# Optimization experiments

Measured on AMD Instinct MI355X. Metric: run time of the kernel, lower is better.

## Reference

```python
import jax, jax.numpy as jnp
import numpy as np

N_NODES = 50000
N_EDGES = 1600000
D_FEAT = 64
N_SCALARS = 4
N_GRAPHS = 64
HIDDEN = 128
OUT = 128


def setup_inputs() -> dict:
    key = jax.random.key(0)
    ks = jax.random.split(key, 8)
    x = jax.random.normal(ks[0], (N_NODES, D_FEAT), dtype=jnp.float32)
    scalars = jax.random.normal(ks[1], (N_GRAPHS, N_SCALARS), dtype=jnp.float32)
    batch = jnp.sort(jax.random.randint(ks[2], (N_NODES,), 0, N_GRAPHS))
    edge_index = jax.random.randint(ks[3], (2, N_EDGES), 0, N_NODES)
    d_in = 2 * (D_FEAT + N_SCALARS)  # 136: EdgeConv-style cat([x_i, x_j - x_i])
    W1 = jax.random.normal(ks[4], (d_in, HIDDEN), dtype=jnp.float32) * (1.0 / np.sqrt(d_in))
    b1 = jnp.zeros((HIDDEN,), dtype=jnp.float32)
    W2 = jax.random.normal(ks[5], (HIDDEN, OUT), dtype=jnp.float32) * (1.0 / np.sqrt(HIDDEN))
    b2 = jnp.zeros((OUT,), dtype=jnp.float32)
    return {"x": x, "scalars": scalars, "batch": batch, "edge_index": edge_index,
            "W1": W1, "b1": b1, "W2": W2, "b2": b2}


def reference(x, scalars, batch, edge_index, W1, b1, W2, b2):
    # _reshape_scalars: gather per-graph scalars to nodes via batch index
    s = scalars[batch]                       # [N, n_scalars]
    h = jnp.concatenate([x, s], axis=-1)     # [N, d_feat + n_scalars]
    src, dst = edge_index[0], edge_index[1]  # edge j -> i (PyG convention)
    h_i = h[dst]                             # target node features [E, F]
    h_j = h[src]                             # source node features [E, F]
    m_in = jnp.concatenate([h_i, h_j - h_i], axis=-1)  # [E, 2F]
    m = jax.nn.relu(m_in @ W1 + b1) @ W2 + b2          # edge MLP [E, OUT]
    out = jax.ops.segment_sum(m, dst, num_segments=x.shape[0])  # add-aggregation
    return out
```

## Files before the change

kernel.cpp:

```cpp
#include <hip/hip_runtime.h>

#define N_NODES   50000
#define N_EDGES   1600000
#define D_FEAT    64
#define N_SCALARS 4
#define HIDDEN    128
#define OUT_DIM   128
#define UV_DIM    256

#define SLICE_SH  6
#define SLICE_N   (1 << SLICE_SH)
#define NSLICE    ((N_NODES + SLICE_N - 1) >> SLICE_SH)
#define CAP       2560
#define CAPN      80
#define CAPN_DW   (CAPN / 2)
#define CHUNK     4096

#define N_WAVES   (N_NODES / 16)
#define G1_BLOCKS ((N_WAVES + 3) / 4)
#define BIN_BLOCKS ((N_EDGES + CHUNK - 1) / CHUNK)
#define AGG_BLOCKS (N_NODES / 16)

typedef __attribute__((ext_vector_type(8))) _Float16 half8;
typedef __attribute__((ext_vector_type(2))) _Float16 half2v;
typedef __attribute__((ext_vector_type(4))) float    f32x4;

__device__ __forceinline__ float wf_elem(const float* W1, int k, int j) {
    float wb = W1[(k + 68) * HIDDEN + (j & 127)];
    return (j < HIDDEN) ? (W1[k * HIDDEN + j] - wb) : wb;
}

__device__ __forceinline__ unsigned char f2bf8(float f) {
    unsigned short h = __builtin_bit_cast(unsigned short, (_Float16)f);
    unsigned r = ((unsigned)h + 0x7Fu + ((h >> 8) & 1u)) >> 8;
    return (unsigned char)r;
}

__device__ __forceinline__ half2v bf8x2_to_h2(unsigned short w) {
    unsigned r = __builtin_amdgcn_perm(0u, (unsigned)w, 0x010C000Cu);
    return __builtin_bit_cast(half2v, r);
}

__global__ __launch_bounds__(256) void prep_kernel(
    const float* __restrict__ W1, const float* __restrict__ b1,
    const float* __restrict__ W2, const float* __restrict__ scalars,
    _Float16* __restrict__ WfT, _Float16* __restrict__ W2T,
    float* __restrict__ SG, int* __restrict__ tails)
{
    const int idx = blockIdx.x * 256 + threadIdx.x;
    {   int j = idx >> 6, k = idx & 63;
        WfT[idx] = (_Float16)wf_elem(W1, k, j); }
    {   int j = idx >> 7, k = idx & 127;
        W2T[idx] = (_Float16)W2[k * OUT_DIM + j]; }
    {   int g = idx >> 8, j = idx & 255;
        float s = (j < HIDDEN) ? b1[j] : 0.f;
        #pragma unroll
        for (int t = 0; t < N_SCALARS; ++t)
            s = fmaf(scalars[g * N_SCALARS + t], wf_elem(W1, D_FEAT + t, j), s);
        SG[idx] = s; }
    if (idx < NSLICE) tails[idx] = 0;
}

__global__ __launch_bounds__(256) void gemm1_bin(
    const float* __restrict__ x, const int* __restrict__ batch,
    const _Float16* __restrict__ WfT, const float* __restrict__ SG,
    _Float16* __restrict__ Uh, unsigned char* __restrict__ Vb8,
    const int* __restrict__ ei, int* __restrict__ tails,
    unsigned* __restrict__ glist)
{
    __shared__ unsigned buf[CHUNK];
    __shared__ int hist[NSLICE];
    __shared__ int binStart[NSLICE];
    __shared__ int cursor[NSLICE];
    __shared__ int gbase[NSLICE];
    __shared__ int scanTmp[256];

    const int tid = threadIdx.x;

    if (blockIdx.x < G1_BLOCKS) {
        const int wid = (blockIdx.x * 256 + tid) >> 6;
        if (wid >= N_WAVES) return;
        const int lane = tid & 63;
        const int quad = lane >> 4;
        const int l15  = lane & 15;
        const int row0 = wid * 16;

        f32x4 acc[16];
        #pragma unroll
        for (int c = 0; c < 16; ++c) { f32x4 z = {0.f,0.f,0.f,0.f}; acc[c] = z; }

        const float* xrow = x + (row0 + l15) * D_FEAT;
        #pragma unroll
        for (int t = 0; t < 2; ++t) {
            const int k0 = 32 * t + quad * 8;
            float4 a0 = *(const float4*)(xrow + k0);
            float4 a1 = *(const float4*)(xrow + k0 + 4);
            half8 af;
            af[0] = (_Float16)a0.x; af[1] = (_Float16)a0.y;
            af[2] = (_Float16)a0.z; af[3] = (_Float16)a0.w;
            af[4] = (_Float16)a1.x; af[5] = (_Float16)a1.y;
            af[6] = (_Float16)a1.z; af[7] = (_Float16)a1.w;
            #pragma unroll
            for (int c = 0; c < 16; ++c) {
                half8 bf = *(const half8*)(WfT + (c * 16 + l15) * 64 + k0);
                acc[c] = __builtin_amdgcn_mfma_f32_16x16x32_f16(af, bf, acc[c], 0, 0, 0);
            }
        }

        const int gA = batch[row0];
        const int gB = batch[row0 + 15];

        if (gA == gB) {
            const float* SGr = SG + gA * UV_DIM;
            #pragma unroll
            for (int c = 0; c < 16; ++c) {
                const int col = c * 16 + l15;
                const float sg = SGr[col];
                #pragma unroll
                for (int j = 0; j < 4; ++j) {
                    const int n = row0 + quad * 4 + j;
                    float v = acc[c][j] + sg;
                    if (col < HIDDEN) Uh[(n << 7) + col] = (_Float16)v;
                    else              Vb8[(n << 7) + col - HIDDEN] = f2bf8(v);
                }
            }
        } else {
            int bg[4];
            #pragma unroll
            for (int j = 0; j < 4; ++j) bg[j] = batch[row0 + quad * 4 + j];
            #pragma unroll
            for (int c = 0; c < 16; ++c) {
                const int col = c * 16 + l15;
                #pragma unroll
                for (int j = 0; j < 4; ++j) {
                    const int n = row0 + quad * 4 + j;
                    float v = acc[c][j] + SG[bg[j] * UV_DIM + col];
                    if (col < HIDDEN) Uh[(n << 7) + col] = (_Float16)v;
                    else              Vb8[(n << 7) + col - HIDDEN] = f2bf8(v);
                }
            }
        }
        return;
    }

    const int e0  = (blockIdx.x - G1_BLOCKS) * CHUNK;
    const int nE  = min(CHUNK, N_EDGES - e0);

    for (int i = tid; i < NSLICE; i += 256) hist[i] = 0;
    __syncthreads();

    unsigned ent[CHUNK / 256];
    #pragma unroll
    for (int j = 0; j < CHUNK / 256; ++j) {
        int e = e0 + tid + j * 256;
        if (e < N_EDGES) {
            unsigned s = (unsigned)ei[e];
            unsigned d = (unsigned)ei[N_EDGES + e];
            ent[j] = (d << 16) | s;
            atomicAdd(&hist[d >> SLICE_SH], 1);
        } else {
            ent[j] = 0xFFFFFFFFu;
        }
    }
    __syncthreads();

    const int base4 = tid * 4;
    int loc[4];
    int sum = 0;
    #pragma unroll
    for (int k = 0; k < 4; ++k) {
        int b = base4 + k;
        loc[k] = (b < NSLICE) ? hist[b] : 0;
        sum += loc[k];
    }
    scanTmp[tid] = sum;
    __syncthreads();
    for (int d = 1; d < 256; d <<= 1) {
        int v = (tid >= d) ? scanTmp[tid - d] : 0;
        __syncthreads();
        scanTmp[tid] += v;
        __syncthreads();
    }
    int run = (tid == 0) ? 0 : scanTmp[tid - 1];
    #pragma unroll
    for (int k = 0; k < 4; ++k) {
        int b = base4 + k;
        if (b < NSLICE) { binStart[b] = run; cursor[b] = run; run += loc[k]; }
    }
    __syncthreads();

    #pragma unroll
    for (int j = 0; j < CHUNK / 256; ++j) {
        if (ent[j] != 0xFFFFFFFFu) {
            int sl = (int)(ent[j] >> (16 + SLICE_SH));
            int pos = atomicAdd(&cursor[sl], 1);
            buf[pos] = ent[j];
        }
    }
    __syncthreads();

    for (int s = tid; s < NSLICE; s += 256) {
        int c = hist[s];
        if (c > 0) gbase[s] = atomicAdd(&tails[s], c);
    }
    __syncthreads();

    for (int i = tid; i < nE; i += 256) {
        unsigned e = buf[i];
        int sl = (int)(e >> (16 + SLICE_SH));
        int di = gbase[sl] + (i - binStart[sl]);
        if (di < CAP) glist[(size_t)sl * CAP + di] = e;
    }
}

__global__ __launch_bounds__(256) void rebin_kernel(
    const unsigned* glist, const int* __restrict__ tails,
    unsigned short* nlist, int* __restrict__ degN)
{
    __shared__ unsigned short lists[64 * CAPN];
    __shared__ int cur[64];

    const int sl  = blockIdx.x;
    const int tid = threadIdx.x;
    const unsigned* lst = glist + (size_t)sl * CAP;
    const int cnt = min(tails[sl], CAP);

    if (tid < 64) cur[tid] = 0;
    __syncthreads();

    for (int i = tid; i < cnt; i += 256) {
        unsigned e = lst[i];
        int b = (e >> 16) & 63;
        int pos = atomicAdd(&cur[b], 1);
        if (pos < CAPN) lists[b * CAPN + pos] = (unsigned short)e;
    }
    __syncthreads();

    unsigned* N32 = (unsigned*)nlist + (size_t)sl * (64 * CAPN_DW);
    const unsigned* L32 = (const unsigned*)lists;
    #pragma unroll
    for (int k = 0; k < (64 * CAPN_DW) / 256; ++k)
        N32[tid + k * 256] = L32[tid + k * 256];

    if (tid < 64) degN[sl * 64 + tid] = min(cur[tid], CAPN);
}

__global__ __launch_bounds__(256) void agg_gemm2(
    const unsigned short* __restrict__ nlist, const int* __restrict__ degN,
    const _Float16* __restrict__ Uh, const unsigned char* __restrict__ Vb8,
    const _Float16* __restrict__ W2T, const float* __restrict__ b2,
    float* __restrict__ out)
{
    __shared__ _Float16 aggA[16][136];
    __shared__ int deg16[16];

    const int node0 = blockIdx.x << 4;
    const int tid   = threadIdx.x;
    const int wave  = tid >> 6;
    const int lane  = tid & 63;
    const int quad  = lane >> 4;
    const int l15   = lane & 15;
    const int c2    = lane * 2;
    const half2v zero = {(_Float16)0, (_Float16)0};

    if (tid < 16) deg16[tid] = min(degN[node0 + tid], CAPN);

#define VLOAD(s) (*(const unsigned short*)(Vb8 + ((size_t)(s) << 7) + c2))

    #pragma unroll
    for (int i = 0; i < 4; ++i) {
        const int b  = wave * 4 + i;
        const int nu = __builtin_amdgcn_readfirstlane(node0 + b);
        const int deg = min(degN[nu], CAPN);
        const unsigned* Lw = (const unsigned*)nlist + (size_t)nu * CAPN_DW;
        half2v u2 = *(const half2v*)(Uh + ((size_t)nu << 7) + c2);
        half2v acc2 = zero;

        const int nf = deg >> 4;
        for (int ch = 0; ch < nf; ++ch) {
            const unsigned* Lc = Lw + ch * 8;
            unsigned d0 = Lc[0], d1 = Lc[1], d2 = Lc[2], d3 = Lc[3];
            unsigned d4 = Lc[4], d5 = Lc[5], d6 = Lc[6], d7 = Lc[7];
            unsigned short w0  = VLOAD(d0 & 0xFFFFu), w1  = VLOAD(d0 >> 16);
            unsigned short w2  = VLOAD(d1 & 0xFFFFu), w3  = VLOAD(d1 >> 16);
            unsigned short w4  = VLOAD(d2 & 0xFFFFu), w5  = VLOAD(d2 >> 16);
            unsigned short w6  = VLOAD(d3 & 0xFFFFu), w7  = VLOAD(d3 >> 16);
            unsigned short w8  = VLOAD(d4 & 0xFFFFu), w9  = VLOAD(d4 >> 16);
            unsigned short w10 = VLOAD(d5 & 0xFFFFu), w11 = VLOAD(d5 >> 16);
            unsigned short w12 = VLOAD(d6 & 0xFFFFu), w13 = VLOAD(d6 >> 16);
            unsigned short w14 = VLOAD(d7 & 0xFFFFu), w15 = VLOAD(d7 >> 16);
            half2v m0  = __builtin_elementwise_max(u2 + bf8x2_to_h2(w0),  zero);
            half2v m1  = __builtin_elementwise_max(u2 + bf8x2_to_h2(w1),  zero);
            half2v m2  = __builtin_elementwise_max(u2 + bf8x2_to_h2(w2),  zero);
            half2v m3  = __builtin_elementwise_max(u2 + bf8x2_to_h2(w3),  zero);
            half2v m4  = __builtin_elementwise_max(u2 + bf8x2_to_h2(w4),  zero);
            half2v m5  = __builtin_elementwise_max(u2 + bf8x2_to_h2(w5),  zero);
            half2v m6  = __builtin_elementwise_max(u2 + bf8x2_to_h2(w6),  zero);
            half2v m7  = __builtin_elementwise_max(u2 + bf8x2_to_h2(w7),  zero);
            half2v m8  = __builtin_elementwise_max(u2 + bf8x2_to_h2(w8),  zero);
            half2v m9  = __builtin_elementwise_max(u2 + bf8x2_to_h2(w9),  zero);
            half2v m10 = __builtin_elementwise_max(u2 + bf8x2_to_h2(w10), zero);
            half2v m11 = __builtin_elementwise_max(u2 + bf8x2_to_h2(w11), zero);
            half2v m12 = __builtin_elementwise_max(u2 + bf8x2_to_h2(w12), zero);
            half2v m13 = __builtin_elementwise_max(u2 + bf8x2_to_h2(w13), zero);
            half2v m14 = __builtin_elementwise_max(u2 + bf8x2_to_h2(w14), zero);
            half2v m15 = __builtin_elementwise_max(u2 + bf8x2_to_h2(w15), zero);
            half2v s0 = (m0 + m1) + (m2 + m3);
            half2v s1 = (m4 + m5) + (m6 + m7);
            half2v s2 = (m8 + m9) + (m10 + m11);
            half2v s3 = (m12 + m13) + (m14 + m15);
            acc2 += (s0 + s1) + (s2 + s3);
        }
        const int rem = deg & 15;
        if (rem) {
            const unsigned* Lc = Lw + nf * 8;
            for (int e = 0; e < rem; ++e) {
                unsigned dw = Lc[e >> 1];
                unsigned s = (e & 1) ? (dw >> 16) : (dw & 0xFFFFu);
                unsigned short w = VLOAD(s);
                acc2 += __builtin_elementwise_max(u2 + bf8x2_to_h2(w), zero);
            }
        }
        *(half2v*)&aggA[b][c2] = acc2;
    }
#undef VLOAD
    __syncthreads();

    f32x4 accm[2];
    {   f32x4 z = {0.f,0.f,0.f,0.f}; accm[0] = z; accm[1] = z; }
    #pragma unroll
    for (int t = 0; t < 4; ++t) {
        const int k0 = 32 * t + quad * 8;
        half8 af = *(const half8*)&aggA[l15][k0];
        #pragma unroll
        for (int c = 0; c < 2; ++c) {
            const int ct = wave * 2 + c;
            half8 bf = *(const half8*)(W2T + ((ct * 16 + l15) << 7) + k0);
            accm[c] = __builtin_amdgcn_mfma_f32_16x16x32_f16(af, bf, accm[c], 0, 0, 0);
        }
    }
    int dgj[4];
    #pragma unroll
    for (int j = 0; j < 4; ++j) dgj[j] = deg16[quad * 4 + j];

    #pragma unroll
    for (int c = 0; c < 2; ++c) {
        const int col = (wave * 2 + c) * 16 + l15;
        const float bb = b2[col];
        #pragma unroll
        for (int j = 0; j < 4; ++j) {
            const int n = node0 + quad * 4 + j;
            out[(size_t)n * OUT_DIM + col] = accm[c][j] + bb * (float)dgj[j];
        }
    }
}

extern "C" void kernel_launch(void* const* d_in, const int* in_sizes, int n_in,
                              void* d_out, int out_size, void* d_ws, size_t ws_size,
                              hipStream_t stream)
{
    const float* x       = (const float*)d_in[0];
    const float* scalars = (const float*)d_in[1];
    const int*   batch   = (const int*)d_in[2];
    const int*   ei      = (const int*)d_in[3];
    const float* W1      = (const float*)d_in[4];
    const float* b1      = (const float*)d_in[5];
    const float* W2      = (const float*)d_in[6];
    const float* b2      = (const float*)d_in[7];
    float*       out     = (float*)d_out;

    _Float16*       Uh    = (_Float16*)d_ws;
    unsigned char*  Vb8   = (unsigned char*)(Uh + (size_t)N_NODES * HIDDEN);
    unsigned*       glist = (unsigned*)(Vb8 + (size_t)N_NODES * HIDDEN);
    unsigned short* nlist = (unsigned short*)glist;
    int*            degN  = (int*)(glist + (size_t)NSLICE * CAP);
    _Float16*       WfT   = (_Float16*)(degN + NSLICE * SLICE_N);
    _Float16*       W2T   = WfT + 256 * 64;
    float*          SG    = (float*)(W2T + 128 * 128);
    int*            tails = (int*)(SG + 64 * UV_DIM);

    prep_kernel<<<64, 256, 0, stream>>>(W1, b1, W2, scalars, WfT, W2T, SG, tails);

    gemm1_bin<<<G1_BLOCKS + BIN_BLOCKS, 256, 0, stream>>>(
        x, batch, WfT, SG, Uh, Vb8, ei, tails, glist);

    rebin_kernel<<<NSLICE, 256, 0, stream>>>(glist, tails, nlist, degN);

    agg_gemm2<<<AGG_BLOCKS, 256, 0, stream>>>(
        nlist, degN, Uh, Vb8, W2T, b2, out);
}
```

Before: 180.3 us.

## Restructure edge aggregation into 16-byte gathers with sentinel-padded neighbor lists

The aggregation kernel now has each wave handle four nodes at once. Groups of 8 lanes each gather a full 128-byte fp8 row with 16-byte loads, and a cross-lane shuffle reduction follows, replacing the old 2-byte-per-lane gathers with a separate remainder loop. Neighbor lists are prefilled with a sentinel node whose fp8 row decodes to a large negative value, so padded slots contribute zero after ReLU and no tail loop is needed. The rebin pass also orders sources in two halves to improve cache locality of the gathers. The cost is extra padded work up to the maximum degree among the four nodes, plus a second pass over each slice's edge list in rebin.

```diff
diff --git a/kernel.cpp b/kernel.cpp
--- a/kernel.cpp
+++ b/kernel.cpp
@@ -15,6 +15,8 @@
 #define CAPN      80
 #define CAPN_DW   (CAPN / 2)
 #define CHUNK     4096
+#define SENTINEL  50000
+#define SRC_HALF  25000
 
 #define N_WAVES   (N_NODES / 16)
 #define G1_BLOCKS ((N_WAVES + 3) / 4)
@@ -36,16 +38,25 @@
     return (unsigned char)r;
 }
 
-__device__ __forceinline__ half2v bf8x2_to_h2(unsigned short w) {
-    unsigned r = __builtin_amdgcn_perm(0u, (unsigned)w, 0x010C000Cu);
-    return __builtin_bit_cast(half2v, r);
+__device__ __forceinline__ half2v bf8lo(unsigned v) {
+    return __builtin_bit_cast(half2v, __builtin_amdgcn_perm(0u, v, 0x010C000Cu));
+}
+__device__ __forceinline__ half2v bf8hi(unsigned v) {
+    return __builtin_bit_cast(half2v, __builtin_amdgcn_perm(0u, v, 0x030C020Cu));
+}
+__device__ __forceinline__ half2v h2bc(unsigned v) {
+    return __builtin_bit_cast(half2v, v);
+}
+__device__ __forceinline__ unsigned h2u(half2v v) {
+    return __builtin_bit_cast(unsigned, v);
 }
 
 __global__ __launch_bounds__(256) void prep_kernel(
     const float* __restrict__ W1, const float* __restrict__ b1,
     const float* __restrict__ W2, const float* __restrict__ scalars,
     _Float16* __restrict__ WfT, _Float16* __restrict__ W2T,
-    float* __restrict__ SG, int* __restrict__ tails)
+    float* __restrict__ SG, int* __restrict__ tails,
+    unsigned char* __restrict__ Vb8)
 {
     const int idx = blockIdx.x * 256 + threadIdx.x;
     {   int j = idx >> 6, k = idx & 63;
@@ -59,6 +70,8 @@
             s = fmaf(scalars[g * N_SCALARS + t], wf_elem(W1, D_FEAT + t, j), s);
         SG[idx] = s; }
     if (idx < NSLICE) tails[idx] = 0;
+    if (idx < 32)
+        ((unsigned*)(Vb8 + (size_t)SENTINEL * HIDDEN))[idx] = 0xFCFCFCFCu;
 }
 
 __global__ __launch_bounds__(256) void gemm1_bin(
@@ -225,19 +238,33 @@
     const unsigned* lst = glist + (size_t)sl * CAP;
     const int cnt = min(tails[sl], CAP);
 
+    unsigned* L32 = (unsigned*)lists;
+    #pragma unroll
+    for (int k = 0; k < (64 * CAPN_DW) / 256; ++k)
+        L32[tid + k * 256] = (SENTINEL << 16) | SENTINEL;
     if (tid < 64) cur[tid] = 0;
     __syncthreads();
 
     for (int i = tid; i < cnt; i += 256) {
         unsigned e = lst[i];
-        int b = (e >> 16) & 63;
-        int pos = atomicAdd(&cur[b], 1);
-        if (pos < CAPN) lists[b * CAPN + pos] = (unsigned short)e;
+        if ((e & 0xFFFFu) < SRC_HALF) {
+            int b = (e >> 16) & 63;
+            int pos = atomicAdd(&cur[b], 1);
+            if (pos < CAPN) lists[b * CAPN + pos] = (unsigned short)e;
+        }
+    }
+    __syncthreads();
+    for (int i = tid; i < cnt; i += 256) {
+        unsigned e = lst[i];
+        if ((e & 0xFFFFu) >= SRC_HALF) {
+            int b = (e >> 16) & 63;
+            int pos = atomicAdd(&cur[b], 1);
+            if (pos < CAPN) lists[b * CAPN + pos] = (unsigned short)e;
+        }
     }
     __syncthreads();
 
     unsigned* N32 = (unsigned*)nlist + (size_t)sl * (64 * CAPN_DW);
-    const unsigned* L32 = (const unsigned*)lists;
     #pragma unroll
     for (int k = 0; k < (64 * CAPN_DW) / 256; ++k)
         N32[tid + k * 256] = L32[tid + k * 256];
@@ -258,74 +285,90 @@
     const int tid   = threadIdx.x;
     const int wave  = tid >> 6;
     const int lane  = tid & 63;
-    const int quad  = lane >> 4;
-    const int l15   = lane & 15;
-    const int c2    = lane * 2;
+    const int g     = lane >> 3;
+    const int co    = (lane & 7) * 16;
     const half2v zero = {(_Float16)0, (_Float16)0};
 
     if (tid < 16) deg16[tid] = min(degN[node0 + tid], CAPN);
 
-#define VLOAD(s) (*(const unsigned short*)(Vb8 + ((size_t)(s) << 7) + c2))
-
+    const int nbase = node0 + wave * 4;
+    int dg[4];
+    #pragma unroll
+    for (int i = 0; i < 4; ++i) dg[i] = min(degN[nbase + i], CAPN);
+    const int nch = (max(max(dg[0], dg[1]), max(dg[2], dg[3])) + 7) >> 3;
+
+    const unsigned char* Vbc = Vb8 + co;
+    const unsigned short* Lp[4];
+    #pragma unroll
+    for (int i = 0; i < 4; ++i)
+        Lp[i] = nlist + (size_t)(nbase + i) * CAPN + g;
+
+    half2v U[4][8], A[4][8];
     #pragma unroll
     for (int i = 0; i < 4; ++i) {
-        const int b  = wave * 4 + i;
-        const int nu = __builtin_amdgcn_readfirstlane(node0 + b);
-        const int deg = min(degN[nu], CAPN);
-        const unsigned* Lw = (const unsigned*)nlist + (size_t)nu * CAPN_DW;
-        half2v u2 = *(const half2v*)(Uh + ((size_t)nu << 7) + c2);
-        half2v acc2 = zero;
-
-        const int nf = deg >> 4;
-        for (int ch = 0; ch < nf; ++ch) {
-            const unsigned* Lc = Lw + ch * 8;
-            unsigned d0 = Lc[0], d1 = Lc[1], d2 = Lc[2], d3 = Lc[3];
-            unsigned d4 = Lc[4], d5 = Lc[5], d6 = Lc[6], d7 = Lc[7];
-            unsigned short w0  = VLOAD(d0 & 0xFFFFu), w1  = VLOAD(d0 >> 16);
-            unsigned short w2  = VLOAD(d1 & 0xFFFFu), w3  = VLOAD(d1 >> 16);
-            unsigned short w4  = VLOAD(d2 & 0xFFFFu), w5  = VLOAD(d2 >> 16);
-            unsigned short w6  = VLOAD(d3 & 0xFFFFu), w7  = VLOAD(d3 >> 16);
-            unsigned short w8  = VLOAD(d4 & 0xFFFFu), w9  = VLOAD(d4 >> 16);
-            unsigned short w10 = VLOAD(d5 & 0xFFFFu), w11 = VLOAD(d5 >> 16);
-            unsigned short w12 = VLOAD(d6 & 0xFFFFu), w13 = VLOAD(d6 >> 16);
-            unsigned short w14 = VLOAD(d7 & 0xFFFFu), w15 = VLOAD(d7 >> 16);
-            half2v m0  = __builtin_elementwise_max(u2 + bf8x2_to_h2(w0),  zero);
-            half2v m1  = __builtin_elementwise_max(u2 + bf8x2_to_h2(w1),  zero);
-            half2v m2  = __builtin_elementwise_max(u2 + bf8x2_to_h2(w2),  zero);
-            half2v m3  = __builtin_elementwise_max(u2 + bf8x2_to_h2(w3),  zero);
-            half2v m4  = __builtin_elementwise_max(u2 + bf8x2_to_h2(w4),  zero);
-            half2v m5  = __builtin_elementwise_max(u2 + bf8x2_to_h2(w5),  zero);
-            half2v m6  = __builtin_elementwise_max(u2 + bf8x2_to_h2(w6),  zero);
-            half2v m7  = __builtin_elementwise_max(u2 + bf8x2_to_h2(w7),  zero);
-            half2v m8  = __builtin_elementwise_max(u2 + bf8x2_to_h2(w8),  zero);
-            half2v m9  = __builtin_elementwise_max(u2 + bf8x2_to_h2(w9),  zero);
-            half2v m10 = __builtin_elementwise_max(u2 + bf8x2_to_h2(w10), zero);
-            half2v m11 = __builtin_elementwise_max(u2 + bf8x2_to_h2(w11), zero);
-            half2v m12 = __builtin_elementwise_max(u2 + bf8x2_to_h2(w12), zero);
-            half2v m13 = __builtin_elementwise_max(u2 + bf8x2_to_h2(w13), zero);
-            half2v m14 = __builtin_elementwise_max(u2 + bf8x2_to_h2(w14), zero);
-            half2v m15 = __builtin_elementwise_max(u2 + bf8x2_to_h2(w15), zero);
-            half2v s0 = (m0 + m1) + (m2 + m3);
-            half2v s1 = (m4 + m5) + (m6 + m7);
-            half2v s2 = (m8 + m9) + (m10 + m11);
-            half2v s3 = (m12 + m13) + (m14 + m15);
-            acc2 += (s0 + s1) + (s2 + s3);
-        }
-        const int rem = deg & 15;
-        if (rem) {
-            const unsigned* Lc = Lw + nf * 8;
-            for (int e = 0; e < rem; ++e) {
-                unsigned dw = Lc[e >> 1];
-                unsigned s = (e & 1) ? (dw >> 16) : (dw & 0xFFFFu);
-                unsigned short w = VLOAD(s);
-                acc2 += __builtin_elementwise_max(u2 + bf8x2_to_h2(w), zero);
-            }
-        }
-        *(half2v*)&aggA[b][c2] = acc2;
-    }
-#undef VLOAD
-    __syncthreads();
-
+        const _Float16* up = Uh + (((size_t)(nbase + i)) << 7) + co;
+        uint4 a = *(const uint4*)up;
+        uint4 b = *(const uint4*)(up + 8);
+        U[i][0] = h2bc(a.x); U[i][1] = h2bc(a.y);
+        U[i][2] = h2bc(a.z); U[i][3] = h2bc(a.w);
+        U[i][4] = h2bc(b.x); U[i][5] = h2bc(b.y);
+        U[i][6] = h2bc(b.z); U[i][7] = h2bc(b.w);
+        #pragma unroll
+        for (int k = 0; k < 8; ++k) A[i][k] = zero;
+    }
+
+    unsigned sidc[4];
+    #pragma unroll
+    for (int i = 0; i < 4; ++i) sidc[i] = Lp[i][0];
+
+    for (int ch = 0; ch < nch; ++ch) {
+        uint4 v[4];
+        #pragma unroll
+        for (int i = 0; i < 4; ++i)
+            v[i] = *(const uint4*)(Vbc + ((size_t)sidc[i] << 7));
+        unsigned sidn[4];
+        #pragma unroll
+        for (int i = 0; i < 4; ++i) sidn[i] = Lp[i][(ch + 1) * 8];
+        #pragma unroll
+        for (int i = 0; i < 4; ++i) {
+            A[i][0] += __builtin_elementwise_max(U[i][0] + bf8lo(v[i].x), zero);
+            A[i][1] += __builtin_elementwise_max(U[i][1] + bf8hi(v[i].x), zero);
+            A[i][2] += __builtin_elementwise_max(U[i][2] + bf8lo(v[i].y), zero);
+            A[i][3] += __builtin_elementwise_max(U[i][3] + bf8hi(v[i].y), zero);
+            A[i][4] += __builtin_elementwise_max(U[i][4] + bf8lo(v[i].z), zero);
+            A[i][5] += __builtin_elementwise_max(U[i][5] + bf8hi(v[i].z), zero);
+            A[i][6] += __builtin_elementwise_max(U[i][6] + bf8lo(v[i].w), zero);
+            A[i][7] += __builtin_elementwise_max(U[i][7] + bf8hi(v[i].w), zero);
+            sidc[i] = sidn[i];
+        }
+    }
+
+    #pragma unroll
+    for (int i = 0; i < 4; ++i) {
+        #pragma unroll
+        for (int k = 0; k < 8; ++k) {
+            half2v t = A[i][k];
+            t += h2bc((unsigned)__shfl_xor((int)h2u(t), 8));
+            t += h2bc((unsigned)__shfl_xor((int)h2u(t), 16));
+            t += h2bc((unsigned)__shfl_xor((int)h2u(t), 32));
+            A[i][k] = t;
+        }
+    }
+
+    if (lane < 8) {
+        #pragma unroll
+        for (int i = 0; i < 4; ++i) {
+            _Float16* dst = &aggA[wave * 4 + i][co];
+            uint4 w0 = { h2u(A[i][0]), h2u(A[i][1]), h2u(A[i][2]), h2u(A[i][3]) };
+            uint4 w1 = { h2u(A[i][4]), h2u(A[i][5]), h2u(A[i][6]), h2u(A[i][7]) };
+            *(uint4*)dst = w0;
+            *(uint4*)(dst + 8) = w1;
+        }
+    }
+    __syncthreads();
+
+    const int quad = lane >> 4;
+    const int l15  = lane & 15;
     f32x4 accm[2];
     {   f32x4 z = {0.f,0.f,0.f,0.f}; accm[0] = z; accm[1] = z; }
     #pragma unroll
@@ -371,7 +414,7 @@
 
     _Float16*       Uh    = (_Float16*)d_ws;
     unsigned char*  Vb8   = (unsigned char*)(Uh + (size_t)N_NODES * HIDDEN);
-    unsigned*       glist = (unsigned*)(Vb8 + (size_t)N_NODES * HIDDEN);
+    unsigned*       glist = (unsigned*)(Vb8 + (size_t)(N_NODES + 1) * HIDDEN);
     unsigned short* nlist = (unsigned short*)glist;
     int*            degN  = (int*)(glist + (size_t)NSLICE * CAP);
     _Float16*       WfT   = (_Float16*)(degN + NSLICE * SLICE_N);
@@ -379,7 +422,7 @@
     float*          SG    = (float*)(W2T + 128 * 128);
     int*            tails = (int*)(SG + 64 * UV_DIM);
 
-    prep_kernel<<<64, 256, 0, stream>>>(W1, b1, W2, scalars, WfT, W2T, SG, tails);
+    prep_kernel<<<64, 256, 0, stream>>>(W1, b1, W2, scalars, WfT, W2T, SG, tails, Vb8);
 
     gemm1_bin<<<G1_BLOCKS + BIN_BLOCKS, 256, 0, stream>>>(
         x, batch, WfT, SG, Uh, Vb8, ei, tails, glist);
```

Result: faster. 168.5 us (-6.5%).
